# Optimization experiments

Hardware: AMD Instinct MI355X
Metric: run time of the kernel (lower is better)

Reference implementation:

```python
import jax, jax.numpy as jnp
import numpy as np

B = 4
NV = 6890           # SMPL vertex count
NF0 = 13776         # SMPL face count (before fill_back)
T = 3               # tex_size
IMG = 128           # render image size
UVH = UVW = 256     # uv image resolution
FLENGTH = 500.0
NEAR, FAR = 0.1, 25.0
CHUNK = 128         # faces per z-buffer scan step
BIG = jnp.float32(1e10)


def setup_inputs():
    key = jax.random.key(0)
    ks = jax.random.split(key, 5)
    faces0 = jax.random.randint(ks[0], (NF0, 3), 0, NV, dtype=jnp.int32)
    faces = jnp.concatenate([faces0, faces0[:, ::-1]], axis=0)  # fill_back
    cam = jnp.concatenate([0.8 + 0.2 * jax.random.uniform(ks[1], (B, 1)),
                           0.05 * jax.random.normal(ks[2], (B, 2))], axis=1)
    vertices = 0.3 * jax.random.normal(ks[3], (B, NV, 3))
    uv_imgs = jax.random.uniform(ks[4], (B, 3, UVH, UVW))
    img2uv_sampler = jax.random.uniform(jax.random.fold_in(key, 7),
                                        (faces.shape[0], T * T, 2)) * 2.0 - 1.0
    return {"cam": cam, "vertices": vertices, "uv_imgs": uv_imgs,
            "img2uv_sampler": img2uv_sampler, "faces": faces}


def _grid_sample(img, grid):
    # img (B,C,H,W), grid (B,N,2) xy in [-1,1]; bilinear, align_corners=False, zeros padding
    Bc, C, H, W = img.shape
    x = (grid[..., 0] + 1.0) * (W * 0.5) - 0.5
    y = (grid[..., 1] + 1.0) * (H * 0.5) - 0.5
    x0f = jnp.floor(x); y0f = jnp.floor(y)
    wx = x - x0f; wy = y - y0f
    x0 = x0f.astype(jnp.int32); y0 = y0f.astype(jnp.int32)
    imgf = img.reshape(Bc, C, H * W)
    def gat(yi, xi, w):
        valid = (xi >= 0) & (xi < W) & (yi >= 0) & (yi < H)
        idx = jnp.clip(yi, 0, H - 1) * W + jnp.clip(xi, 0, W - 1)
        v = jax.vmap(lambda im, i: im[:, i])(imgf, idx)  # (B,C,N)
        return v * (w * valid)[:, None, :]
    return (gat(y0, x0, (1 - wx) * (1 - wy)) + gat(y0, x0 + 1, wx * (1 - wy)) +
            gat(y0 + 1, x0, (1 - wx) * wy) + gat(y0 + 1, x0 + 1, wx * wy))


def _extract_tex(uv_imgs, sampler, nf):
    # sampler (B,nf,T*T,2) -> textures (B,nf,T,T,T,3)
    tex = _grid_sample(uv_imgs, sampler.reshape(uv_imgs.shape[0], -1, 2))
    tex = tex.reshape(-1, 3, nf, T, T).transpose(0, 2, 3, 4, 1)  # (B,nf,T,T,3)
    return jnp.broadcast_to(tex[:, :, :, :, None, :], tex.shape[:4] + (T, 3))


def _lighting(face_verts, textures):
    # module defaults: ambient intensity 1, directional 0, white lights, dir=(0,1,0)
    v0, v1, v2 = face_verts[:, :, 0], face_verts[:, :, 1], face_verts[:, :, 2]
    n = jnp.cross(v1 - v0, v2 - v0)
    n = n / (jnp.linalg.norm(n, axis=-1, keepdims=True) + 1e-10)
    cos = jnp.maximum(n @ jnp.array([0.0, 1.0, 0.0]), 0.0)       # (B,F)
    light = 1.0 * jnp.ones(3) + 0.0 * cos[..., None] * jnp.ones(3)  # (B,F,3)
    return textures * light[:, :, None, None, None, :]


def _weak_projection(cam, vertices):
    p = IMG / 2.0
    tz = FLENGTH / (p * cam[:, 0:1])                              # (B,1)
    v2d = cam[:, None, 0:1] * (vertices[:, :, :2] + cam[:, None, 1:])
    return jnp.concatenate([v2d, vertices[:, :, 2:3] + tz[:, None, :]], axis=-1)


def _bary(fv, px, py):
    # fv: (...,3,3) triangle screen verts; px,py broadcastable pixel coords
    x0 = fv[..., 0, 0]; y0 = fv[..., 0, 1]
    x1 = fv[..., 1, 0]; y1 = fv[..., 1, 1]
    x2 = fv[..., 2, 0]; y2 = fv[..., 2, 1]
    w0 = (x2 - x1) * (py - y1) - (y2 - y1) * (px - x1)
    w1 = (x0 - x2) * (py - y2) - (y0 - y2) * (px - x2)
    w2 = (x1 - x0) * (py - y0) - (y1 - y0) * (px - x0)
    area = w0 + w1 + w2
    s = jnp.where(area == 0, 1.0, area)
    return w0 / s, w1 / s, w2 / s, area


def _pixel_grid():
    xs = (2.0 * jnp.arange(IMG) + 1.0) / IMG - 1.0                # (W,)
    ys = (1.0 - (2.0 * jnp.arange(IMG) + 1.0) / IMG)[:, None]     # (H,1), +y up
    return xs, ys


def _rasterize_fim(face_verts):
    # face_verts (B,F,3,3) in screen coords -> face index map (B,H,W), -1 = bg
    Bc, F = face_verts.shape[:2]
    pad = (-F) % CHUNK
    fv = jnp.pad(face_verts, ((0, 0), (0, pad), (0, 0), (0, 0)))
    S = (F + pad) // CHUNK
    fv = fv.reshape(Bc, S, CHUNK, 3, 3).transpose(1, 0, 2, 3, 4)  # (S,B,C,3,3)
    xs, ys = _pixel_grid()
    def step(carry, inp):
        zbuf, fim = carry
        f, base = inp
        fe = f[:, :, None, None, :, :]                            # (B,C,1,1,3,3)
        b0, b1, b2, area = _bary(fe, xs, ys)                      # (B,C,H,W)
        z0 = f[:, :, 0, 2][..., None, None]
        z1 = f[:, :, 1, 2][..., None, None]
        z2 = f[:, :, 2, 2][..., None, None]
        invz = b0 / z0 + b1 / z1 + b2 / z2                        # perspective-correct
        zp = 1.0 / jnp.where(invz == 0, 1.0, invz)
        inside = (b0 >= 0) & (b1 >= 0) & (b2 >= 0) & (area > 0)   # front-facing only
        valid = inside & (zp > NEAR) & (zp < FAR)
        depth = jnp.where(valid, zp, BIG)
        dmin = jnp.min(depth, axis=1)                             # (B,H,W)
        amin = jnp.argmin(depth, axis=1).astype(jnp.int32) + base
        better = dmin < zbuf
        return (jnp.where(better, dmin, zbuf),
                jnp.where(better, amin, fim)), None
    zbuf0 = jnp.full((Bc, IMG, IMG), BIG)
    fim0 = jnp.full((Bc, IMG, IMG), -1, jnp.int32)
    bases = (jnp.arange(S) * CHUNK).astype(jnp.int32)
    (zbuf, fim), _ = jax.lax.scan(step, (zbuf0, fim0), (fv, bases))
    return fim


def _shade(face_verts, textures, fim):
    # nearest-texel barycentric texture lookup, as in neural_renderer forward
    Bc, F = face_verts.shape[:2]
    fid = jnp.clip(fim, 0, F - 1).reshape(Bc, -1)                 # (B,HW)
    fv = jax.vmap(lambda v, i: v[i])(face_verts, fid)             # (B,HW,3,3)
    fv = fv.reshape(Bc, IMG, IMG, 3, 3)
    xs, ys = _pixel_grid()
    b0, b1, b2, _ = _bary(fv, xs, ys)                             # (B,H,W)
    t0 = jnp.clip(jnp.floor(b0 * T).astype(jnp.int32), 0, T - 1)
    t1 = jnp.clip(jnp.floor(b1 * T).astype(jnp.int32), 0, T - 1)
    t2 = jnp.clip(jnp.floor(b2 * T).astype(jnp.int32), 0, T - 1)
    idx = ((jnp.clip(fim, 0, F - 1) * T + t0) * T + t1) * T + t2  # (B,H,W)
    texf = textures.reshape(Bc, F * T * T * T, 3)
    col = jax.vmap(lambda t, i: t[i])(texf, idx.reshape(Bc, -1))  # (B,HW,3)
    col = col.reshape(Bc, IMG, IMG, 3)
    col = jnp.where((fim >= 0)[..., None], col, 0.0)              # bg color (0,0,0)
    return col.transpose(0, 3, 1, 2)                              # (B,3,H,W)


def reference(cam, vertices, uv_imgs, img2uv_sampler, faces):
    Bc = cam.shape[0]
    nf = faces.shape[0]
    sampler = jnp.broadcast_to(img2uv_sampler[None], (Bc,) + img2uv_sampler.shape)
    textures = _extract_tex(uv_imgs, sampler, nf)                 # (B,nf,T,T,T,3)
    textures = _lighting(vertices[:, faces], textures)
    verts_p = _weak_projection(cam, vertices)
    fv = verts_p[:, faces]                                        # (B,nf,3,3)
    fv_sg = jax.lax.stop_gradient(fv)  # hard rasterization is non-differentiable
    fim = _rasterize_fim(fv_sg)
    images = _shade(fv_sg, textures, fim)
    return images


if __name__ == "__main__":
    out = reference(**setup_inputs())
    print(out.shape, out.dtype)
```

## Files before the change

kernel.cpp:

```cpp
#include <hip/hip_runtime.h>
#include <stdint.h>

#pragma clang fp contract(off)

#define B_    4
#define NV_   6890
#define NF_   27552
#define IMG_  128
#define UV_   256
#define NPIX  (IMG_*IMG_)

#define TS_     8
#define TPB_    (IMG_/TS_)
#define NTILE_  (TPB_*TPB_)
#define NBIN_   (B_*NTILE_)
#define LIST_CAP (2*1024*1024)
#define MAXC_   (LIST_CAP/256 + NBIN_)

__global__ void __launch_bounds__(256) project_k(
    const float* __restrict__ cam, const float* __restrict__ verts,
    float* __restrict__ vp) {
  int idx = blockIdx.x * 256 + threadIdx.x;
  if (idx >= B_ * NV_) return;
  int b = idx / NV_;
  float c0 = cam[b * 3 + 0], c1 = cam[b * 3 + 1], c2 = cam[b * 3 + 2];
  float tz = 500.0f / (64.0f * c0);
  const float* src = verts + (size_t)idx * 3;
  float* dst = vp + (size_t)idx * 3;
  dst[0] = c0 * (src[0] + c1);
  dst[1] = c0 * (src[1] + c2);
  dst[2] = src[2] + tz;
}

__device__ __forceinline__ int face_tiles(
    const float* __restrict__ vp, const int* __restrict__ faces, int b, int f,
    int& tx0, int& tx1, int& ty0, int& ty1) {
  int ia = faces[f * 3 + 0], ib = faces[f * 3 + 1], ic = faces[f * 3 + 2];
  const float* vb = vp + (size_t)b * NV_ * 3;
  float x0 = vb[ia * 3 + 0], y0 = vb[ia * 3 + 1];
  float x1 = vb[ib * 3 + 0], y1 = vb[ib * 3 + 1];
  float x2 = vb[ic * 3 + 0], y2 = vb[ic * 3 + 1];
  float area_c = (x1 - x0) * (y2 - y0) - (y1 - y0) * (x2 - x0);
  if (area_c < -1e-3f) return 0;
  float xmn = fminf(x0, fminf(x1, x2)), xmx = fmaxf(x0, fmaxf(x1, x2));
  float ymn = fminf(y0, fminf(y1, y2)), ymx = fmaxf(y0, fmaxf(y1, y2));
  int jlo = (int)floorf((xmn + 1.0f) * 64.0f - 0.5f) - 1;
  int jhi = (int)ceilf ((xmx + 1.0f) * 64.0f - 0.5f) + 1;
  int ilo = (int)floorf((1.0f - ymx) * 64.0f - 0.5f) - 1;
  int ihi = (int)ceilf ((1.0f - ymn) * 64.0f - 0.5f) + 1;
  if (jhi < 0 || ihi < 0 || jlo > IMG_ - 1 || ilo > IMG_ - 1) return 0;
  jlo = max(jlo, 0); ilo = max(ilo, 0);
  jhi = min(jhi, IMG_ - 1); ihi = min(ihi, IMG_ - 1);
  tx0 = jlo >> 3; tx1 = jhi >> 3; ty0 = ilo >> 3; ty1 = ihi >> 3;
  return 1;
}

__global__ void __launch_bounds__(256) bin_count_k(
    const float* __restrict__ vp, const int* __restrict__ faces,
    int* __restrict__ cnt, int* __restrict__ rects) {
  __shared__ int scnt[NTILE_];
  int f = blockIdx.x * 256 + threadIdx.x;
  int b = blockIdx.y;
  scnt[threadIdx.x] = 0;
  __syncthreads();
  int tx0, tx1, ty0, ty1;
  int valid = (f < NF_) ? face_tiles(vp, faces, b, f, tx0, tx1, ty0, ty1) : 0;
  if (f < NF_)
    rects[(size_t)b * NF_ + f] =
        valid ? (tx0 | (tx1 << 4) | (ty0 << 8) | (ty1 << 12) | (1 << 16)) : 0;
  if (valid)
    for (int ty = ty0; ty <= ty1; ++ty)
      for (int tx = tx0; tx <= tx1; ++tx)
        atomicAdd(&scnt[ty * TPB_ + tx], 1);
  __syncthreads();
  int t = threadIdx.x;
  int v = scnt[t];
  if (v > 0) atomicAdd(&cnt[b * NTILE_ + t], v);
}

__global__ void __launch_bounds__(1024) scan_k(
    const int* __restrict__ cnt, int* __restrict__ off, int* __restrict__ cur,
    int* __restrict__ work, int* __restrict__ nC) {
  __shared__ int sm[NBIN_];
  int t = threadIdx.x;
  int v = cnt[t];
  sm[t] = v;
  __syncthreads();
  for (int d = 1; d < NBIN_; d <<= 1) {
    int u = (t >= d) ? sm[t - d] : 0;
    __syncthreads();
    sm[t] += u;
    __syncthreads();
  }
  int o = sm[t] - v;
  off[t] = o;
  cur[t] = o;
  int nch = (v + 255) >> 8;
  __syncthreads();
  sm[t] = nch;
  __syncthreads();
  for (int d = 1; d < NBIN_; d <<= 1) {
    int u = (t >= d) ? sm[t - d] : 0;
    __syncthreads();
    sm[t] += u;
    __syncthreads();
  }
  int cb = sm[t] - nch;
  if (t == NBIN_ - 1) nC[0] = sm[t];
  for (int c = 0; c < nch; ++c) work[cb + c] = t | (c << 10);
}

__global__ void __launch_bounds__(256) bin_fill_k(
    const int* __restrict__ rects, int* __restrict__ cur,
    int* __restrict__ list) {
  __shared__ int scnt[NTILE_];
  __shared__ int sbase[NTILE_];
  int f = blockIdx.x * 256 + threadIdx.x;
  int b = blockIdx.y;
  scnt[threadIdx.x] = 0;
  __syncthreads();
  int rv = (f < NF_) ? rects[(size_t)b * NF_ + f] : 0;
  int valid = rv >> 16;
  int tx0 = rv & 15, tx1 = (rv >> 4) & 15;
  int ty0 = (rv >> 8) & 15, ty1 = (rv >> 12) & 15;
  if (valid)
    for (int ty = ty0; ty <= ty1; ++ty)
      for (int tx = tx0; tx <= tx1; ++tx)
        atomicAdd(&scnt[ty * TPB_ + tx], 1);
  __syncthreads();
  int t = threadIdx.x;
  int v = scnt[t];
  if (v > 0) sbase[t] = atomicAdd(&cur[b * NTILE_ + t], v);
  __syncthreads();
  scnt[t] = 0;
  __syncthreads();
  if (valid)
    for (int ty = ty0; ty <= ty1; ++ty)
      for (int tx = tx0; tx <= tx1; ++tx) {
        int bin = ty * TPB_ + tx;
        int r = atomicAdd(&scnt[bin], 1);
        int slot = sbase[bin] + r;
        if (slot < LIST_CAP) list[slot] = f;
      }
}

__global__ void __launch_bounds__(256) raster_k(
    const float* __restrict__ vp, const int* __restrict__ faces,
    const int* __restrict__ list, const int* __restrict__ cnt,
    const int* __restrict__ off, const int* __restrict__ work,
    const int* __restrict__ nC, unsigned long long* __restrict__ zkey) {
  __shared__ float4 fd[4][5][64];
  __shared__ unsigned long long mg[4][64];
  int bid = blockIdx.x;
  if (bid >= nC[0]) return;
  int wkv = work[bid];
  int bin = wkv & (NBIN_ - 1);
  int chunk = wkv >> 10;
  int b = bin >> 8;
  int t = bin & 255;
  int tyT = t >> 4, txT = t & 15;
  int ws = threadIdx.x >> 6, lane = threadIdx.x & 63;
  int pi = tyT * TS_ + (lane >> 3);
  int pj = txT * TS_ + (lane & 7);
  float px = fmaf((float)pj, 0.015625f, -0.9921875f);
  float py = fmaf((float)pi, -0.015625f, 0.9921875f);

  int n = cnt[bin];
  int seg = (chunk << 8) + (ws << 6);
  int base0 = off[bin] + seg;
  int mw = min(n - seg, 64);
  mw = max(mw, 0);

  if (lane < mw) {
    int fid = list[base0 + lane];
    int ia = faces[fid * 3 + 0], ib = faces[fid * 3 + 1],
        ic = faces[fid * 3 + 2];
    const float* vb = vp + (size_t)b * NV_ * 3;
    float X0 = vb[ia * 3 + 0], Y0 = vb[ia * 3 + 1], Z0 = vb[ia * 3 + 2];
    float X1 = vb[ib * 3 + 0], Y1 = vb[ib * 3 + 1], Z1 = vb[ib * 3 + 2];
    float X2 = vb[ic * 3 + 0], Y2 = vb[ic * 3 + 1], Z2 = vb[ic * 3 + 2];
    fd[ws][0][lane] = make_float4(X2 - X1, Y2 - Y1, X1, Y1);
    fd[ws][1][lane] = make_float4(X0 - X2, Y0 - Y2, X2, Y2);
    fd[ws][2][lane] = make_float4(X1 - X0, Y1 - Y0, X0, Y0);
    fd[ws][3][lane] = make_float4(Z0, Z1, Z2, __int_as_float(fid));
    fd[ws][4][lane] =
        make_float4(Z1 * Z2, Z0 * Z2, Z0 * Z1, Z0 * Z1 * Z2);
  }
  __syncthreads();

  unsigned long long kb = ~0ull;
  float gate = __uint_as_float(0xFFFFFFFFu);
  for (int q = 0; q < mw; ++q) {
    float4 A = fd[ws][0][q];
    float4 Bv = fd[ws][1][q];
    float4 Cv = fd[ws][2][q];
    float w0 = A.x * (py - A.w) - A.y * (px - A.z);
    float w1 = Bv.x * (py - Bv.w) - Bv.y * (px - Bv.z);
    float w2 = Cv.x * (py - Cv.w) - Cv.y * (px - Cv.z);
    float area = (w0 + w1) + w2;
    float mn = fminf(w0, fminf(w1, w2));
    if (area > 0.0f && !(mn < 0.0f)) {
      float4 P = fd[ws][4][q];
      float num = (w0 * P.x + w1 * P.y) + w2 * P.z;
      float zpa = (area * P.w) * __builtin_amdgcn_rcpf(num);
      if (!(zpa > gate)) {
        float4 Z = fd[ws][3][q];
        float b0 = w0 / area, b1 = w1 / area, b2 = w2 / area;
        float invz = (b0 / Z.x + b1 / Z.y) + b2 / Z.z;
        float zp = 1.0f / (invz == 0.0f ? 1.0f : invz);
        if (zp > 0.1f && zp < 25.0f) {
          unsigned long long key =
              ((unsigned long long)__float_as_uint(zp) << 32) |
              (unsigned int)__float_as_int(Z.w);
          if (key < kb) {
            kb = key;
            gate = __uint_as_float((unsigned int)(kb >> 32)) * 1.001f;
          }
        }
      }
    }
  }

  mg[ws][lane] = kb;
  __syncthreads();
  if (ws == 0) {
    unsigned long long k0 = mg[0][lane];
    unsigned long long k1 = mg[1][lane];
    unsigned long long k2 = mg[2][lane];
    unsigned long long k3 = mg[3][lane];
    k0 = k1 < k0 ? k1 : k0;
    k2 = k3 < k2 ? k3 : k2;
    k0 = k2 < k0 ? k2 : k0;
    if (k0 != ~0ull)
      atomicMin(zkey + (size_t)b * NPIX + pi * IMG_ + pj, k0);
  }
}

#define TAP(ty, tx, wexpr)                                                   \
  {                                                                          \
    int ty_ = (ty), tx_ = (tx);                                              \
    float w_ = (wexpr);                                                      \
    float valid_ =                                                           \
        (tx_ >= 0 && tx_ < UV_ && ty_ >= 0 && ty_ < UV_) ? 1.0f : 0.0f;      \
    float wv_ = w_ * valid_;                                                 \
    int cy_ = min(max(ty_, 0), UV_ - 1), cx_ = min(max(tx_, 0), UV_ - 1);    \
    int o_ = cy_ * UV_ + cx_;                                                \
    cr = cr + img[o_] * wv_;                                                 \
    cg = cg + img[UV_ * UV_ + o_] * wv_;                                     \
    cb = cb + img[2 * UV_ * UV_ + o_] * wv_;                                 \
  }

__global__ void __launch_bounds__(256) shade_k(
    const float* __restrict__ vp, const int* __restrict__ faces,
    const float* __restrict__ uv, const float* __restrict__ samp,
    const unsigned long long* __restrict__ zkey, float* __restrict__ out) {
  int idx = blockIdx.x * 256 + threadIdx.x;
  if (idx >= B_ * NPIX) return;
  int b = idx / NPIX;
  int p = idx - b * NPIX;
  int ii = p / IMG_;
  int jj = p - ii * IMG_;

  unsigned long long key = zkey[idx];
  float cr = 0.0f, cg = 0.0f, cb = 0.0f;
  if (key != 0xFFFFFFFFFFFFFFFFull) {
    int f = (int)(key & 0xFFFFFFFFull);
    int ia = faces[f * 3 + 0], ib = faces[f * 3 + 1], ic = faces[f * 3 + 2];
    const float* vb = vp + (size_t)b * NV_ * 3;
    float x0 = vb[ia * 3 + 0], y0 = vb[ia * 3 + 1];
    float x1 = vb[ib * 3 + 0], y1 = vb[ib * 3 + 1];
    float x2 = vb[ic * 3 + 0], y2 = vb[ic * 3 + 1];
    float px = (float)(2 * jj + 1) / 128.0f - 1.0f;
    float py = 1.0f - (float)(2 * ii + 1) / 128.0f;
    float w0 = (x2 - x1) * (py - y1) - (y2 - y1) * (px - x1);
    float w1 = (x0 - x2) * (py - y2) - (y0 - y2) * (px - x2);
    float w2 = (x1 - x0) * (py - y0) - (y1 - y0) * (px - x0);
    float area = (w0 + w1) + w2;
    float s = (area == 0.0f) ? 1.0f : area;
    float b0 = w0 / s, b1 = w1 / s;
    int t0 = min(max((int)floorf(b0 * 3.0f), 0), 2);
    int t1 = min(max((int)floorf(b1 * 3.0f), 0), 2);

    const float* g = samp + ((size_t)f * 9 + (size_t)(t0 * 3 + t1)) * 2;
    float gx = g[0], gy = g[1];
    float x = (gx + 1.0f) * 128.0f - 0.5f;
    float y = (gy + 1.0f) * 128.0f - 0.5f;
    float x0f = floorf(x), y0f = floorf(y);
    float wx = x - x0f, wy = y - y0f;
    int xi = (int)x0f, yi = (int)y0f;
    float omwx = 1.0f - wx, omwy = 1.0f - wy;
    const float* img = uv + (size_t)b * 3 * UV_ * UV_;
    TAP(yi,     xi,     omwx * omwy)
    TAP(yi,     xi + 1, wx * omwy)
    TAP(yi + 1, xi,     omwx * wy)
    TAP(yi + 1, xi + 1, wx * wy)
  }
  out[((size_t)b * 3 + 0) * NPIX + p] = cr;
  out[((size_t)b * 3 + 1) * NPIX + p] = cg;
  out[((size_t)b * 3 + 2) * NPIX + p] = cb;
}

extern "C" void kernel_launch(void* const* d_in, const int* in_sizes, int n_in,
                              void* d_out, int out_size, void* d_ws,
                              size_t ws_size, hipStream_t stream) {
  const float* cam   = (const float*)d_in[0];
  const float* verts = (const float*)d_in[1];
  const float* uv    = (const float*)d_in[2];
  const float* samp  = (const float*)d_in[3];
  const int*   faces = (const int*)d_in[4];

  char* ws = (char*)d_ws;
  size_t o = 0;
  unsigned long long* zkey = (unsigned long long*)(ws + o);
  o += (size_t)B_ * NPIX * 8;
  float* vp = (float*)(ws + o);
  o += ((size_t)B_ * NV_ * 3 * 4 + 1023) & ~1023ull;
  int* cnt   = (int*)(ws + o); o += NBIN_ * 4;
  int* offs  = (int*)(ws + o); o += NBIN_ * 4;
  int* cur   = (int*)(ws + o); o += NBIN_ * 4;
  int* nC    = (int*)(ws + o); o += 1024;
  int* work  = (int*)(ws + o); o += (size_t)MAXC_ * 4;
  int* rects = (int*)(ws + o); o += (size_t)B_ * NF_ * 4;
  int* list  = (int*)(ws + o);

  hipMemsetAsync(zkey, 0xFF, (size_t)B_ * NPIX * 8, stream);
  hipMemsetAsync(cnt, 0, NBIN_ * 4, stream);
  project_k<<<(B_ * NV_ + 255) / 256, 256, 0, stream>>>(cam, verts, vp);
  dim3 bgrid((NF_ + 255) / 256, B_);
  bin_count_k<<<bgrid, 256, 0, stream>>>(vp, faces, cnt, rects);
  scan_k<<<1, NBIN_, 0, stream>>>(cnt, offs, cur, work, nC);
  bin_fill_k<<<bgrid, 256, 0, stream>>>(rects, cur, list);
  raster_k<<<MAXC_, 256, 0, stream>>>(vp, faces, list, cnt, offs, work, nC,
                                      zkey);
  shade_k<<<(B_ * NPIX + 255) / 256, 256, 0, stream>>>(vp, faces, uv, samp,
                                                       zkey, (float*)d_out);
}
```

Before: 214.7 us.

## Sort faces by min depth per wave and early-exit against existing z-buffer

Each wave sorts its 64 candidate faces by minimum vertex depth using a shuffle bitonic sort, then stores them in sorted order. The current depth-buffer value for each pixel is read up front with an atomic and used to seed the depth gate. The face loop stops once every lane's best depth is nearer than the next face's minimum depth. This aims to skip triangle tests that cannot win, at the cost of the sort, an extra atomic per pixel and more shared memory.

```diff
diff --git a/kernel.cpp b/kernel.cpp
--- a/kernel.cpp
+++ b/kernel.cpp
@@ -151,6 +151,8 @@
     const int* __restrict__ nC, unsigned long long* __restrict__ zkey) {
   __shared__ float4 fd[4][5][64];
   __shared__ unsigned long long mg[4][64];
+  __shared__ float zmn[4][64];
+  __shared__ unsigned sdz[64];
   int bid = blockIdx.x;
   if (bid >= nC[0]) return;
   int wkv = work[bid];
@@ -171,26 +173,58 @@
   int mw = min(n - seg, 64);
   mw = max(mw, 0);
 
+  if (threadIdx.x < 64) {
+    unsigned long long s =
+        atomicMin(zkey + (size_t)b * NPIX + pi * IMG_ + pj, ~0ull);
+    sdz[threadIdx.x] = (unsigned)(s >> 32);
+  }
+
+  unsigned skey = 0xFFFFFFC0u | (unsigned)lane;
+  float ztr = 0.0f;
+  int fid = 0;
+  float X0 = 0, Y0 = 0, Z0 = 0, X1 = 0, Y1 = 0, Z1 = 0, X2 = 0, Y2 = 0,
+        Z2 = 0;
   if (lane < mw) {
-    int fid = list[base0 + lane];
+    fid = list[base0 + lane];
     int ia = faces[fid * 3 + 0], ib = faces[fid * 3 + 1],
         ic = faces[fid * 3 + 2];
     const float* vb = vp + (size_t)b * NV_ * 3;
-    float X0 = vb[ia * 3 + 0], Y0 = vb[ia * 3 + 1], Z0 = vb[ia * 3 + 2];
-    float X1 = vb[ib * 3 + 0], Y1 = vb[ib * 3 + 1], Z1 = vb[ib * 3 + 2];
-    float X2 = vb[ic * 3 + 0], Y2 = vb[ic * 3 + 1], Z2 = vb[ic * 3 + 2];
-    fd[ws][0][lane] = make_float4(X2 - X1, Y2 - Y1, X1, Y1);
-    fd[ws][1][lane] = make_float4(X0 - X2, Y0 - Y2, X2, Y2);
-    fd[ws][2][lane] = make_float4(X1 - X0, Y1 - Y0, X0, Y0);
-    fd[ws][3][lane] = make_float4(Z0, Z1, Z2, __int_as_float(fid));
-    fd[ws][4][lane] =
+    X0 = vb[ia * 3 + 0]; Y0 = vb[ia * 3 + 1]; Z0 = vb[ia * 3 + 2];
+    X1 = vb[ib * 3 + 0]; Y1 = vb[ib * 3 + 1]; Z1 = vb[ib * 3 + 2];
+    X2 = vb[ic * 3 + 0]; Y2 = vb[ic * 3 + 1]; Z2 = vb[ic * 3 + 2];
+    float zmin = fminf(Z0, fminf(Z1, Z2));
+    unsigned zb = __float_as_uint(zmin) & 0xFFFFFFC0u;
+    skey = zb | (unsigned)lane;
+    ztr = __uint_as_float(zb);
+  }
+  int rank = lane;
+  int dosort = (mw > 16);
+  if (dosort) {
+    for (int k = 2; k <= 64; k <<= 1)
+      for (int j = k >> 1; j > 0; j >>= 1) {
+        unsigned o = (unsigned)__shfl_xor((int)skey, j, 64);
+        unsigned mn = skey < o ? skey : o;
+        unsigned mx = skey < o ? o : skey;
+        skey = (((lane & k) == 0) == ((lane & j) == 0)) ? mn : mx;
+      }
+    rank = __builtin_amdgcn_ds_permute(((int)(skey & 63u)) << 2, lane);
+  }
+  if (lane < mw) {
+    fd[ws][0][rank] = make_float4(X2 - X1, Y2 - Y1, X1, Y1);
+    fd[ws][1][rank] = make_float4(X0 - X2, Y0 - Y2, X2, Y2);
+    fd[ws][2][rank] = make_float4(X1 - X0, Y1 - Y0, X0, Y0);
+    fd[ws][3][rank] = make_float4(Z0, Z1, Z2, __int_as_float(fid));
+    fd[ws][4][rank] =
         make_float4(Z1 * Z2, Z0 * Z2, Z0 * Z1, Z0 * Z1 * Z2);
+    zmn[ws][rank] = ztr;
   }
   __syncthreads();
 
   unsigned long long kb = ~0ull;
-  float gate = __uint_as_float(0xFFFFFFFFu);
+  float kbz = __uint_as_float(sdz[lane]);
+  float gate = kbz * 1.001f;
   for (int q = 0; q < mw; ++q) {
+    if (dosort && __all(zmn[ws][q] > kbz)) break;
     float4 A = fd[ws][0][q];
     float4 Bv = fd[ws][1][q];
     float4 Cv = fd[ws][2][q];
@@ -214,7 +248,9 @@
               (unsigned int)__float_as_int(Z.w);
           if (key < kb) {
             kb = key;
-            gate = __uint_as_float((unsigned int)(kb >> 32)) * 1.001f;
+            float zacc = __uint_as_float((unsigned)(kb >> 32));
+            kbz = !(zacc >= kbz) ? zacc : kbz;
+            gate = kbz * 1.001f;
           }
         }
       }
```

After: 207.4 us. 3.4% less time.

## Restructure raster into cull, approximate-depth, and exact-resolve passes seeded from zbuffer

Applied to the files above, without the earlier changes.

The raster kernel now first reads the current z-buffer value for its 64 pixels to seed a depth threshold. Faces whose minimum vertex depth exceeds the wavefront-wide threshold are skipped. A first pass finds each pixel's best depth using the cheap reciprocal-based estimate, and a second pass builds a per-lane bitmask of candidate faces near that depth. Only those candidates get the exact divisions for the final key. This aims to cut the expensive division path and loop work, at the cost of two extra passes over the face list and added wavefront reductions and ballots.

```diff
diff --git a/kernel.cpp b/kernel.cpp
--- a/kernel.cpp
+++ b/kernel.cpp
@@ -151,6 +151,8 @@
     const int* __restrict__ nC, unsigned long long* __restrict__ zkey) {
   __shared__ float4 fd[4][5][64];
   __shared__ unsigned long long mg[4][64];
+  __shared__ float zmn[4][64];
+  __shared__ unsigned sdz[64];
   int bid = blockIdx.x;
   if (bid >= nC[0]) return;
   int wkv = work[bid];
@@ -170,6 +172,12 @@
   int base0 = off[bin] + seg;
   int mw = min(n - seg, 64);
   mw = max(mw, 0);
+
+  if (threadIdx.x < 64) {
+    unsigned long long s =
+        atomicMin(zkey + (size_t)b * NPIX + pi * IMG_ + pj, ~0ull);
+    sdz[threadIdx.x] = (unsigned)(s >> 32);
+  }
 
   if (lane < mw) {
     int fid = list[base0 + lane];
@@ -185,12 +193,22 @@
     fd[ws][3][lane] = make_float4(Z0, Z1, Z2, __int_as_float(fid));
     fd[ws][4][lane] =
         make_float4(Z1 * Z2, Z0 * Z2, Z0 * Z1, Z0 * Z1 * Z2);
-  }
-  __syncthreads();
-
-  unsigned long long kb = ~0ull;
-  float gate = __uint_as_float(0xFFFFFFFFu);
+    zmn[ws][lane] = fminf(Z0, fminf(Z1, Z2));
+  }
+  __syncthreads();
+
+  unsigned seed_u = min(sdz[lane], 0x7F800000u);
+  float seedf = __uint_as_float(seed_u);
+  unsigned th1u = seed_u;
+  for (int j = 1; j < 64; j <<= 1) {
+    unsigned o = (unsigned)__shfl_xor((int)th1u, j, 64);
+    th1u = o > th1u ? o : th1u;
+  }
+  float th1f = __uint_as_float(th1u);
+
+  unsigned win_u = 0x7F800000u;
   for (int q = 0; q < mw; ++q) {
+    if (zmn[ws][q] > th1f) continue;
     float4 A = fd[ws][0][q];
     float4 Bv = fd[ws][1][q];
     float4 Cv = fd[ws][2][q];
@@ -199,24 +217,68 @@
     float w2 = Cv.x * (py - Cv.w) - Cv.y * (px - Cv.z);
     float area = (w0 + w1) + w2;
     float mn = fminf(w0, fminf(w1, w2));
-    if (area > 0.0f && !(mn < 0.0f)) {
-      float4 P = fd[ws][4][q];
-      float num = (w0 * P.x + w1 * P.y) + w2 * P.z;
-      float zpa = (area * P.w) * __builtin_amdgcn_rcpf(num);
-      if (!(zpa > gate)) {
-        float4 Z = fd[ws][3][q];
-        float b0 = w0 / area, b1 = w1 / area, b2 = w2 / area;
-        float invz = (b0 / Z.x + b1 / Z.y) + b2 / Z.z;
-        float zp = 1.0f / (invz == 0.0f ? 1.0f : invz);
-        if (zp > 0.1f && zp < 25.0f) {
-          unsigned long long key =
-              ((unsigned long long)__float_as_uint(zp) << 32) |
-              (unsigned int)__float_as_int(Z.w);
-          if (key < kb) {
-            kb = key;
-            gate = __uint_as_float((unsigned int)(kb >> 32)) * 1.001f;
-          }
-        }
+    bool pred = (area > 0.0f) && !(mn < 0.0f);
+    if (!__any(pred)) continue;
+    float4 P = fd[ws][4][q];
+    float num = (w0 * P.x + w1 * P.y) + w2 * P.z;
+    float zpa = (area * P.w) * __builtin_amdgcn_rcpf(num);
+    bool ok = pred && (zpa > 0.1001f) && (zpa < 24.975f);
+    unsigned zb = __float_as_uint(zpa);
+    if (ok && zb < win_u) win_u = zb;
+  }
+
+  unsigned tu = win_u < seed_u ? win_u : seed_u;
+  float thrf = __uint_as_float(tu) * 1.001f;
+  unsigned th2u = tu;
+  for (int j = 1; j < 64; j <<= 1) {
+    unsigned o = (unsigned)__shfl_xor((int)th2u, j, 64);
+    th2u = o > th2u ? o : th2u;
+  }
+  float th2f = __uint_as_float(th2u) * 1.001f;
+
+  unsigned long long qmask = 0ull;
+  for (int q = 0; q < mw; ++q) {
+    if (zmn[ws][q] > th2f) continue;
+    float4 A = fd[ws][0][q];
+    float4 Bv = fd[ws][1][q];
+    float4 Cv = fd[ws][2][q];
+    float w0 = A.x * (py - A.w) - A.y * (px - A.z);
+    float w1 = Bv.x * (py - Bv.w) - Bv.y * (px - Bv.z);
+    float w2 = Cv.x * (py - Cv.w) - Cv.y * (px - Cv.z);
+    float area = (w0 + w1) + w2;
+    float mn = fminf(w0, fminf(w1, w2));
+    bool pred = (area > 0.0f) && !(mn < 0.0f);
+    if (!__any(pred)) continue;
+    float4 P = fd[ws][4][q];
+    float num = (w0 * P.x + w1 * P.y) + w2 * P.z;
+    float zpa = (area * P.w) * __builtin_amdgcn_rcpf(num);
+    bool amb = pred && (!(zpa > thrf) ||
+                        (zpa > 0.09989f && zpa < 0.10011f) ||
+                        (zpa > 24.9724f && zpa < 25.0276f));
+    if (amb) qmask |= 1ull << q;
+  }
+
+  unsigned long long kb = ~0ull;
+  while (__any(qmask != 0ull)) {
+    if (qmask != 0ull) {
+      int q = __ffsll(qmask) - 1;
+      qmask &= qmask - 1;
+      float4 A = fd[ws][0][q];
+      float4 Bv = fd[ws][1][q];
+      float4 Cv = fd[ws][2][q];
+      float4 Z = fd[ws][3][q];
+      float w0 = A.x * (py - A.w) - A.y * (px - A.z);
+      float w1 = Bv.x * (py - Bv.w) - Bv.y * (px - Bv.z);
+      float w2 = Cv.x * (py - Cv.w) - Cv.y * (px - Cv.z);
+      float area = (w0 + w1) + w2;
+      float b0 = w0 / area, b1 = w1 / area, b2 = w2 / area;
+      float invz = (b0 / Z.x + b1 / Z.y) + b2 / Z.z;
+      float zp = 1.0f / (invz == 0.0f ? 1.0f : invz);
+      if (zp > 0.1f && zp < 25.0f) {
+        unsigned long long key =
+            ((unsigned long long)__float_as_uint(zp) << 32) |
+            (unsigned int)__float_as_int(Z.w);
+        if (key < kb) kb = key;
       }
     }
   }
```

After: 242.1 us. 12.8% more time.

## Raster one block per tile with min-depth culling and ballot-compacted face lists

Applied to the files above, without the earlier changes.

Each face's minimum vertex z (top 16 bits) is packed into the bin list entries. The rasterizer now runs one block per tile, and each wavefront loops over the tile's faces in 64-face segments. Faces whose min-depth code exceeds the running per-tile depth threshold are culled, and survivors are compacted by ballot rank. Exact barycentric depth is computed only in a second pass over ambiguous candidates. This drops the chunked work list, the second scan, the zkey memset and the atomicMin in favour of direct stores, at the cost of serialising long bins and adding near/far and approximation edge-case handling.

```diff
diff --git a/kernel.cpp b/kernel.cpp
--- a/kernel.cpp
+++ b/kernel.cpp
@@ -15,7 +15,6 @@
 #define NTILE_  (TPB_*TPB_)
 #define NBIN_   (B_*NTILE_)
 #define LIST_CAP (2*1024*1024)
-#define MAXC_   (LIST_CAP/256 + NBIN_)
 
 __global__ void __launch_bounds__(256) project_k(
     const float* __restrict__ cam, const float* __restrict__ verts,
@@ -34,7 +33,7 @@
 
 __device__ __forceinline__ int face_tiles(
     const float* __restrict__ vp, const int* __restrict__ faces, int b, int f,
-    int& tx0, int& tx1, int& ty0, int& ty1) {
+    int& tx0, int& tx1, int& ty0, int& ty1, unsigned& z16) {
   int ia = faces[f * 3 + 0], ib = faces[f * 3 + 1], ic = faces[f * 3 + 2];
   const float* vb = vp + (size_t)b * NV_ * 3;
   float x0 = vb[ia * 3 + 0], y0 = vb[ia * 3 + 1];
@@ -52,6 +51,8 @@
   jlo = max(jlo, 0); ilo = max(ilo, 0);
   jhi = min(jhi, IMG_ - 1); ihi = min(ihi, IMG_ - 1);
   tx0 = jlo >> 3; tx1 = jhi >> 3; ty0 = ilo >> 3; ty1 = ihi >> 3;
+  float z0 = vb[ia * 3 + 2], z1 = vb[ib * 3 + 2], z2 = vb[ic * 3 + 2];
+  z16 = __float_as_uint(fminf(z0, fminf(z1, z2))) >> 16;
   return 1;
 }
 
@@ -64,10 +65,14 @@
   scnt[threadIdx.x] = 0;
   __syncthreads();
   int tx0, tx1, ty0, ty1;
-  int valid = (f < NF_) ? face_tiles(vp, faces, b, f, tx0, tx1, ty0, ty1) : 0;
+  unsigned z16 = 0;
+  int valid =
+      (f < NF_) ? face_tiles(vp, faces, b, f, tx0, tx1, ty0, ty1, z16) : 0;
   if (f < NF_)
     rects[(size_t)b * NF_ + f] =
-        valid ? (tx0 | (tx1 << 4) | (ty0 << 8) | (ty1 << 12) | (1 << 16)) : 0;
+        valid ? (int)((z16 << 16) | (unsigned)(tx0 | (tx1 << 4) | (ty0 << 8) |
+                                               (ty1 << 12)))
+              : (int)0xFFFF0000u;
   if (valid)
     for (int ty = ty0; ty <= ty1; ++ty)
       for (int tx = tx0; tx <= tx1; ++tx)
@@ -79,8 +84,7 @@
 }
 
 __global__ void __launch_bounds__(1024) scan_k(
-    const int* __restrict__ cnt, int* __restrict__ off, int* __restrict__ cur,
-    int* __restrict__ work, int* __restrict__ nC) {
+    const int* __restrict__ cnt, int* __restrict__ off, int* __restrict__ cur) {
   __shared__ int sm[NBIN_];
   int t = threadIdx.x;
   int v = cnt[t];
@@ -95,19 +99,6 @@
   int o = sm[t] - v;
   off[t] = o;
   cur[t] = o;
-  int nch = (v + 255) >> 8;
-  __syncthreads();
-  sm[t] = nch;
-  __syncthreads();
-  for (int d = 1; d < NBIN_; d <<= 1) {
-    int u = (t >= d) ? sm[t - d] : 0;
-    __syncthreads();
-    sm[t] += u;
-    __syncthreads();
-  }
-  int cb = sm[t] - nch;
-  if (t == NBIN_ - 1) nC[0] = sm[t];
-  for (int c = 0; c < nch; ++c) work[cb + c] = t | (c << 10);
 }
 
 __global__ void __launch_bounds__(256) bin_fill_k(
@@ -119,8 +110,10 @@
   int b = blockIdx.y;
   scnt[threadIdx.x] = 0;
   __syncthreads();
-  int rv = (f < NF_) ? rects[(size_t)b * NF_ + f] : 0;
-  int valid = rv >> 16;
+  unsigned rv =
+      (f < NF_) ? (unsigned)rects[(size_t)b * NF_ + f] : 0xFFFF0000u;
+  unsigned hi = rv >> 16;
+  int valid = (hi != 0xFFFFu);
   int tx0 = rv & 15, tx1 = (rv >> 4) & 15;
   int ty0 = (rv >> 8) & 15, ty1 = (rv >> 12) & 15;
   if (valid)
@@ -134,28 +127,25 @@
   __syncthreads();
   scnt[t] = 0;
   __syncthreads();
-  if (valid)
+  if (valid) {
+    int ev = (int)((hi << 15) | (unsigned)f);
     for (int ty = ty0; ty <= ty1; ++ty)
       for (int tx = tx0; tx <= tx1; ++tx) {
         int bin = ty * TPB_ + tx;
         int r = atomicAdd(&scnt[bin], 1);
         int slot = sbase[bin] + r;
-        if (slot < LIST_CAP) list[slot] = f;
+        if (slot < LIST_CAP) list[slot] = ev;
       }
+  }
 }
 
 __global__ void __launch_bounds__(256) raster_k(
     const float* __restrict__ vp, const int* __restrict__ faces,
     const int* __restrict__ list, const int* __restrict__ cnt,
-    const int* __restrict__ off, const int* __restrict__ work,
-    const int* __restrict__ nC, unsigned long long* __restrict__ zkey) {
+    const int* __restrict__ off, unsigned long long* __restrict__ zkey) {
   __shared__ float4 fd[4][5][64];
   __shared__ unsigned long long mg[4][64];
-  int bid = blockIdx.x;
-  if (bid >= nC[0]) return;
-  int wkv = work[bid];
-  int bin = wkv & (NBIN_ - 1);
-  int chunk = wkv >> 10;
+  int bin = blockIdx.x;
   int b = bin >> 8;
   int t = bin & 255;
   int tyT = t >> 4, txT = t & 15;
@@ -166,59 +156,109 @@
   float py = fmaf((float)pi, -0.015625f, 0.9921875f);
 
   int n = cnt[bin];
-  int seg = (chunk << 8) + (ws << 6);
-  int base0 = off[bin] + seg;
-  int mw = min(n - seg, 64);
-  mw = max(mw, 0);
-
-  if (lane < mw) {
-    int fid = list[base0 + lane];
-    int ia = faces[fid * 3 + 0], ib = faces[fid * 3 + 1],
-        ic = faces[fid * 3 + 2];
-    const float* vb = vp + (size_t)b * NV_ * 3;
-    float X0 = vb[ia * 3 + 0], Y0 = vb[ia * 3 + 1], Z0 = vb[ia * 3 + 2];
-    float X1 = vb[ib * 3 + 0], Y1 = vb[ib * 3 + 1], Z1 = vb[ib * 3 + 2];
-    float X2 = vb[ic * 3 + 0], Y2 = vb[ic * 3 + 1], Z2 = vb[ic * 3 + 2];
-    fd[ws][0][lane] = make_float4(X2 - X1, Y2 - Y1, X1, Y1);
-    fd[ws][1][lane] = make_float4(X0 - X2, Y0 - Y2, X2, Y2);
-    fd[ws][2][lane] = make_float4(X1 - X0, Y1 - Y0, X0, Y0);
-    fd[ws][3][lane] = make_float4(Z0, Z1, Z2, __int_as_float(fid));
-    fd[ws][4][lane] =
-        make_float4(Z1 * Z2, Z0 * Z2, Z0 * Z1, Z0 * Z1 * Z2);
-  }
-  __syncthreads();
+  int base = off[bin];
 
   unsigned long long kb = ~0ull;
-  float gate = __uint_as_float(0xFFFFFFFFu);
-  for (int q = 0; q < mw; ++q) {
-    float4 A = fd[ws][0][q];
-    float4 Bv = fd[ws][1][q];
-    float4 Cv = fd[ws][2][q];
-    float w0 = A.x * (py - A.w) - A.y * (px - A.z);
-    float w1 = Bv.x * (py - Bv.w) - Bv.y * (px - Bv.z);
-    float w2 = Cv.x * (py - Cv.w) - Cv.y * (px - Cv.z);
-    float area = (w0 + w1) + w2;
-    float mn = fminf(w0, fminf(w1, w2));
-    if (area > 0.0f && !(mn < 0.0f)) {
+  unsigned kbz_u = 0x7F800000u;
+  unsigned thr_code = 0xFFFFu;
+  const float* vb = vp + (size_t)b * NV_ * 3;
+
+  for (int seg = ws * 64; seg < n; seg += 256) {
+    int mw = min(n - seg, 64);
+    bool live = false;
+    int fid = 0;
+    if (lane < mw) {
+      unsigned e = (unsigned)list[base + seg + lane];
+      live = ((e >> 15) <= thr_code);
+      fid = (int)(e & 0x7FFFu);
+    }
+    unsigned long long bal = __ballot(live);
+    if (bal == 0ull) continue;
+    int nsurv = (int)__popcll(bal);
+    int rank = (int)__popcll(bal & ((1ull << lane) - 1ull));
+    if (live) {
+      int ia = faces[fid * 3 + 0], ib = faces[fid * 3 + 1],
+          ic = faces[fid * 3 + 2];
+      float X0 = vb[ia * 3 + 0], Y0 = vb[ia * 3 + 1], Z0 = vb[ia * 3 + 2];
+      float X1 = vb[ib * 3 + 0], Y1 = vb[ib * 3 + 1], Z1 = vb[ib * 3 + 2];
+      float X2 = vb[ic * 3 + 0], Y2 = vb[ic * 3 + 1], Z2 = vb[ic * 3 + 2];
+      fd[ws][0][rank] = make_float4(X2 - X1, Y2 - Y1, X1, Y1);
+      fd[ws][1][rank] = make_float4(X0 - X2, Y0 - Y2, X2, Y2);
+      fd[ws][2][rank] = make_float4(X1 - X0, Y1 - Y0, X0, Y0);
+      fd[ws][3][rank] = make_float4(Z0, Z1, Z2, __int_as_float(fid));
+      fd[ws][4][rank] =
+          make_float4(Z1 * Z2, Z0 * Z2, Z0 * Z1, Z0 * Z1 * Z2);
+    }
+
+    unsigned win_u = 0x7F800000u;
+    unsigned long long qm = 0ull;
+    for (int q = 0; q < nsurv; ++q) {
+      float4 A = fd[ws][0][q];
+      float4 Bv = fd[ws][1][q];
+      float4 Cv = fd[ws][2][q];
+      float w0 = A.x * (py - A.w) - A.y * (px - A.z);
+      float w1 = Bv.x * (py - Bv.w) - Bv.y * (px - Bv.z);
+      float w2 = Cv.x * (py - Cv.w) - Cv.y * (px - Cv.z);
+      float area = (w0 + w1) + w2;
+      float mn = fminf(w0, fminf(w1, w2));
+      bool pred = (area > 0.0f) && !(mn < 0.0f);
+      if (!__any(pred)) continue;
       float4 P = fd[ws][4][q];
       float num = (w0 * P.x + w1 * P.y) + w2 * P.z;
       float zpa = (area * P.w) * __builtin_amdgcn_rcpf(num);
-      if (!(zpa > gate)) {
-        float4 Z = fd[ws][3][q];
-        float b0 = w0 / area, b1 = w1 / area, b2 = w2 / area;
-        float invz = (b0 / Z.x + b1 / Z.y) + b2 / Z.z;
-        float zp = 1.0f / (invz == 0.0f ? 1.0f : invz);
-        if (zp > 0.1f && zp < 25.0f) {
-          unsigned long long key =
-              ((unsigned long long)__float_as_uint(zp) << 32) |
-              (unsigned int)__float_as_int(Z.w);
-          if (key < kb) {
-            kb = key;
-            gate = __uint_as_float((unsigned int)(kb >> 32)) * 1.001f;
+      unsigned cu = win_u < kbz_u ? win_u : kbz_u;
+      float thrq = __uint_as_float(cu) * 1.001f;
+      bool amb = pred && (!(zpa > thrq) ||
+                          (zpa > 0.09989f && zpa < 0.10011f) ||
+                          (zpa > 24.9724f && zpa < 25.0276f));
+      if (amb) qm |= 1ull << q;
+      bool ok = pred && (zpa > 0.1001f) && (zpa < 24.975f);
+      unsigned zb = __float_as_uint(zpa);
+      if (ok && zb < win_u) win_u = zb;
+    }
+
+    while (__any(qm != 0ull)) {
+      if (qm != 0ull) {
+        int q = __ffsll(qm) - 1;
+        qm &= qm - 1ull;
+        float4 A = fd[ws][0][q];
+        float4 Bv = fd[ws][1][q];
+        float4 Cv = fd[ws][2][q];
+        float w0 = A.x * (py - A.w) - A.y * (px - A.z);
+        float w1 = Bv.x * (py - Bv.w) - Bv.y * (px - Bv.z);
+        float w2 = Cv.x * (py - Cv.w) - Cv.y * (px - Cv.z);
+        float area = (w0 + w1) + w2;
+        float4 P = fd[ws][4][q];
+        float num = (w0 * P.x + w1 * P.y) + w2 * P.z;
+        float zpa = (area * P.w) * __builtin_amdgcn_rcpf(num);
+        unsigned cu = win_u < kbz_u ? win_u : kbz_u;
+        float thrf = __uint_as_float(cu) * 1.001f;
+        if (!(zpa > thrf) ||
+            (zpa > 0.09989f && zpa < 0.10011f) ||
+            (zpa > 24.9724f && zpa < 25.0276f)) {
+          float4 Z = fd[ws][3][q];
+          float b0 = w0 / area, b1 = w1 / area, b2 = w2 / area;
+          float invz = (b0 / Z.x + b1 / Z.y) + b2 / Z.z;
+          float zp = 1.0f / (invz == 0.0f ? 1.0f : invz);
+          if (zp > 0.1f && zp < 25.0f) {
+            unsigned long long key =
+                ((unsigned long long)__float_as_uint(zp) << 32) |
+                (unsigned int)__float_as_int(Z.w);
+            if (key < kb) {
+              kb = key;
+              kbz_u = (unsigned)(kb >> 32);
+            }
           }
         }
       }
     }
+
+    unsigned mx = kbz_u;
+    for (int j = 1; j < 64; j <<= 1) {
+      unsigned o = (unsigned)__shfl_xor((int)mx, j, 64);
+      mx = o > mx ? o : mx;
+    }
+    thr_code = __float_as_uint(__uint_as_float(mx) * 1.01f) >> 16;
   }
 
   mg[ws][lane] = kb;
@@ -231,8 +271,7 @@
     k0 = k1 < k0 ? k1 : k0;
     k2 = k3 < k2 ? k3 : k2;
     k0 = k2 < k0 ? k2 : k0;
-    if (k0 != ~0ull)
-      atomicMin(zkey + (size_t)b * NPIX + pi * IMG_ + pj, k0);
+    zkey[(size_t)b * NPIX + pi * IMG_ + pj] = k0;
   }
 }
 
@@ -318,20 +357,16 @@
   int* cnt   = (int*)(ws + o); o += NBIN_ * 4;
   int* offs  = (int*)(ws + o); o += NBIN_ * 4;
   int* cur   = (int*)(ws + o); o += NBIN_ * 4;
-  int* nC    = (int*)(ws + o); o += 1024;
-  int* work  = (int*)(ws + o); o += (size_t)MAXC_ * 4;
   int* rects = (int*)(ws + o); o += (size_t)B_ * NF_ * 4;
   int* list  = (int*)(ws + o);
 
-  hipMemsetAsync(zkey, 0xFF, (size_t)B_ * NPIX * 8, stream);
   hipMemsetAsync(cnt, 0, NBIN_ * 4, stream);
   project_k<<<(B_ * NV_ + 255) / 256, 256, 0, stream>>>(cam, verts, vp);
   dim3 bgrid((NF_ + 255) / 256, B_);
   bin_count_k<<<bgrid, 256, 0, stream>>>(vp, faces, cnt, rects);
-  scan_k<<<1, NBIN_, 0, stream>>>(cnt, offs, cur, work, nC);
+  scan_k<<<1, NBIN_, 0, stream>>>(cnt, offs, cur);
   bin_fill_k<<<bgrid, 256, 0, stream>>>(rects, cur, list);
-  raster_k<<<MAXC_, 256, 0, stream>>>(vp, faces, list, cnt, offs, work, nC,
-                                      zkey);
+  raster_k<<<NBIN_, 256, 0, stream>>>(vp, faces, list, cnt, offs, zkey);
   shade_k<<<(B_ * NPIX + 255) / 256, 256, 0, stream>>>(vp, faces, uv, samp,
                                                        zkey, (float*)d_out);
 }
```

Measured after the change: 434.9 us. 103% more time.
